# Performance work log

Hardware: AMD Instinct MI355X
Metric: run time of the kernel (lower is better)

The kernel has to match this reference:

```python
import jax, jax.numpy as jnp
import numpy as np

B, A, C, G = 32, 8732, 201, 50
NEG_TO_POS_RATIO = 3
MIN_NEG_SAMPLES = 0
DET_W, VAL_W = 0.5, 0.5
BOX_W = (10.0, 10.0, 5.0, 5.0)  # torchvision SSD BoxCoder weights


def _rand_boxes(key, shape_prefix):
    k1, k2 = jax.random.split(key)
    cxcy = jax.random.uniform(k1, shape_prefix + (2,)) * 300.0
    wh = jax.random.uniform(k2, shape_prefix + (2,)) * 90.0 + 10.0
    return jnp.concatenate([cxcy - 0.5 * wh, cxcy + 0.5 * wh], axis=-1)


def setup_inputs() -> dict:
    key = jax.random.key(0)
    ks = jax.random.split(key, 8)
    boxes = _rand_boxes(ks[0], (B, G))
    labels = jax.random.randint(ks[1], (B, G), 1, C, dtype=jnp.int32)  # foreground labels > 0
    image_label = jax.random.randint(ks[2], (B,), 0, 2, dtype=jnp.int32)
    bbox_regression = jax.random.normal(ks[3], (B, A, 4), dtype=jnp.float32)
    cls_logits = jax.random.normal(ks[4], (B, A, C), dtype=jnp.float32)
    rejection_logits = jax.random.normal(ks[5], (B, 2), dtype=jnp.float32)
    anchors = _rand_boxes(ks[6], (B, A))
    k7a, k7b = jax.random.split(ks[7])
    fg = jax.random.uniform(k7a, (B, A)) < 0.02
    gt_idx = jax.random.randint(k7b, (B, A), 0, G, dtype=jnp.int32)
    matched_idxs = jnp.where(fg, gt_idx, -1).astype(jnp.int32)
    return {"boxes": boxes, "labels": labels, "image_label": image_label,
            "bbox_regression": bbox_regression, "cls_logits": cls_logits,
            "rejection_logits": rejection_logits, "anchors": anchors,
            "matched_idxs": matched_idxs}


def _encode(gt, anc):
    # torchvision BoxCoder.encode_single with weights (10,10,5,5); boxes are xyxy
    aw = anc[..., 2] - anc[..., 0]
    ah = anc[..., 3] - anc[..., 1]
    acx = anc[..., 0] + 0.5 * aw
    acy = anc[..., 1] + 0.5 * ah
    gw = gt[..., 2] - gt[..., 0]
    gh = gt[..., 3] - gt[..., 1]
    gcx = gt[..., 0] + 0.5 * gw
    gcy = gt[..., 1] + 0.5 * gh
    wx, wy, ww, wh = BOX_W
    return jnp.stack([wx * (gcx - acx) / aw,
                      wy * (gcy - acy) / ah,
                      ww * jnp.log(gw / aw),
                      wh * jnp.log(gh / ah)], axis=-1)


def _forward(boxes, bbox_regression, cls_logits, rejection_logits, anchors,
             labels, image_label, matched_idxs):
    fg = matched_idxs >= 0                                  # [B,A]
    safe = jnp.clip(matched_idxs, 0)                        # in-range gather idx
    num_foreground = fg.sum()

    mg_boxes = jnp.take_along_axis(boxes, safe[..., None], axis=1)  # [B,A,4]
    target_reg = _encode(mg_boxes, anchors)
    d = bbox_regression - target_reg
    ad = jnp.abs(d)
    sl1 = jnp.where(ad < 1.0, 0.5 * d * d, ad - 0.5)        # beta=1.0
    bbox_loss = jnp.sum(sl1 * fg[..., None].astype(sl1.dtype), axis=(1, 2))  # [B]

    # --- classification targets + per-anchor CE ---
    cls_targets = jnp.where(fg, jnp.take_along_axis(labels, safe, axis=1), 0)  # [B,A]
    logp = jax.nn.log_softmax(cls_logits, axis=-1)
    cls_loss = -jnp.take_along_axis(logp, cls_targets[..., None], axis=-1)[..., 0]  # [B,A]

    # --- hard negative mining via double-argsort ranking ---
    fg_mask = cls_targets > 0
    num_neg = NEG_TO_POS_RATIO * fg_mask.sum(axis=1, keepdims=True)
    num_neg = jnp.where(num_neg == 0, MIN_NEG_SAMPLES, num_neg)
    neg_loss = jnp.where(fg_mask, -jnp.inf, cls_loss)
    rank = jnp.argsort(jnp.argsort(-neg_loss, axis=1), axis=1)  # descending rank
    bg_mask = rank < num_neg

    N = jnp.maximum(1, num_foreground).astype(cls_loss.dtype)
    images_without_boxes = (cls_targets.sum(axis=1) == 0).sum()
    N_neg = (MIN_NEG_SAMPLES * images_without_boxes).astype(cls_loss.dtype)

    regression_loss = bbox_loss.sum() / N
    classification_loss = (jnp.sum(jnp.where(fg_mask, cls_loss, 0.0)) +
                           jnp.sum(jnp.where(bg_mask, cls_loss, 0.0))) / (N + N_neg)

    # --- validation head loss ---
    val_logp = jax.nn.log_softmax(rejection_logits, axis=-1)
    validation_loss = -jnp.take_along_axis(val_logp, image_label[:, None], axis=-1).mean()

    loss = DET_W * (regression_loss + classification_loss) + VAL_W * validation_loss
    return jnp.stack([loss, regression_loss, classification_loss, validation_loss])


def reference(boxes, labels, image_label, bbox_regression, cls_logits,
              rejection_logits, anchors, matched_idxs):
    return _forward(boxes, bbox_regression, cls_logits, rejection_logits, anchors,
                    labels, image_label, matched_idxs)
```

## Files before the change

### kernel.cpp

```cpp
#include <hip/hip_runtime.h>
#include <math.h>

#define Bn 32
#define An 8732
#define Cn 201
#define Gn 50

#define APB 16
#define CLS_BLOCKS ((An + APB - 1) / APB)
#define LOG2E 1.44269504088896340736f

__device__ __forceinline__ unsigned int f2key(float f) {
    unsigned int u = __float_as_uint(f);
    return (u & 0x80000000u) ? ~u : (u | 0x80000000u);
}
__device__ __forceinline__ float key2f(unsigned int k) {
    return (k & 0x80000000u) ? __uint_as_float(k & 0x7FFFFFFFu) : __uint_as_float(~k);
}
__device__ __forceinline__ float smooth_l1(float d) {
    float ad = fabsf(d);
    return ad < 1.0f ? 0.5f * d * d : ad - 0.5f;
}

#define FGKEY 0x007FFFFFu

__global__ __launch_bounds__(256) void cls_kernel(
        const float* __restrict__ cls_logits,
        const int*   __restrict__ matched_idxs,
        const int*   __restrict__ labels,
        const float* __restrict__ boxes,
        const float* __restrict__ anchors,
        const float* __restrict__ bbox_regression,
        float* __restrict__ neg_loss,
        float* __restrict__ part_cls,
        float* __restrict__ part_box) {
    __shared__ float shc[4], shb[4];
    int b   = blockIdx.y;
    int grp = threadIdx.x >> 4;
    int sub = threadIdx.x & 15;
    int a   = blockIdx.x * APB + grp;
    bool valid = (a < An);
    size_t row = (size_t)b * An + a;

    float my_cl = 0.f, my_box = 0.f;
    if (valid) {
        const float* lg = cls_logits + row * (size_t)Cn;
        float v[13];
        #pragma unroll
        for (int j = 0; j < 12; ++j) v[j] = lg[sub + 16 * j];
        v[12] = (sub < Cn - 192) ? lg[sub + 192] : -INFINITY;

        float mx = v[0];
        #pragma unroll
        for (int j = 1; j < 13; ++j) mx = fmaxf(mx, v[j]);
        #pragma unroll
        for (int off = 8; off; off >>= 1) mx = fmaxf(mx, __shfl_xor(mx, off, 64));

        float s = 0.f;
        #pragma unroll
        for (int j = 0; j < 13; ++j) s += exp2f((v[j] - mx) * LOG2E);
        #pragma unroll
        for (int off = 8; off; off >>= 1) s += __shfl_xor(s, off, 64);

        if (sub == 0) {
            float lse = mx + logf(s);
            int   mi  = matched_idxs[row];
            bool  fg  = (mi >= 0);
            int   t   = fg ? labels[b * Gn + mi] : 0;
            float cl  = lse - lg[t];
            if (fg) {
                neg_loss[row] = -INFINITY;
                my_cl = cl;
                const float* gt = boxes           + (size_t)(b * Gn + mi) * 4;
                const float* an = anchors         + row * 4;
                const float* rg = bbox_regression + row * 4;
                float aw  = an[2] - an[0], ah  = an[3] - an[1];
                float acx = an[0] + 0.5f * aw, acy = an[1] + 0.5f * ah;
                float gw  = gt[2] - gt[0], gh  = gt[3] - gt[1];
                float gcx = gt[0] + 0.5f * gw, gcy = gt[1] + 0.5f * gh;
                float t0 = 10.f * (gcx - acx) / aw;
                float t1 = 10.f * (gcy - acy) / ah;
                float t2 = 5.f * logf(gw / aw);
                float t3 = 5.f * logf(gh / ah);
                my_box = smooth_l1(rg[0] - t0) + smooth_l1(rg[1] - t1)
                       + smooth_l1(rg[2] - t2) + smooth_l1(rg[3] - t3);
            } else {
                neg_loss[row] = cl;
            }
        }
    }
    my_cl  += __shfl_xor(my_cl, 16, 64);  my_cl  += __shfl_xor(my_cl, 32, 64);
    my_box += __shfl_xor(my_box, 16, 64); my_box += __shfl_xor(my_box, 32, 64);
    int wv = threadIdx.x >> 6, lane = threadIdx.x & 63;
    if (lane == 0) { shc[wv] = my_cl; shb[wv] = my_box; }
    __syncthreads();
    if (threadIdx.x == 0) {
        part_cls[b * CLS_BLOCKS + blockIdx.x] = shc[0] + shc[1] + shc[2] + shc[3];
        part_box[b * CLS_BLOCKS + blockIdx.x] = shb[0] + shb[1] + shb[2] + shb[3];
    }
}

#define MIT 9
__global__ __launch_bounds__(1024) void mining_kernel(
        const float* __restrict__ neg_loss,
        const float* __restrict__ part_cls,
        const float* __restrict__ part_box,
        int*   __restrict__ fg_count,
        float* __restrict__ fg_cls_sum,
        float* __restrict__ bbox_sum,
        float* __restrict__ topk_batch) {
    int b    = blockIdx.x;
    int tid  = threadIdx.x;
    int lane = tid & 63;
    int wv   = tid >> 6;
    __shared__ int   h[256];
    __shared__ float wfa[16], wfb[16];
    __shared__ int   wia[16];
    __shared__ unsigned int sh_prefix;
    __shared__ int sh_krem, sh_k;

    const float* vals = neg_loss + (size_t)b * An;
    unsigned int key[MIT];
    int myfg = 0;
    #pragma unroll
    for (int j = 0; j < MIT; ++j) {
        int i = tid + j * 1024;
        unsigned int kk = 0u;
        if (i < An) { kk = f2key(vals[i]); myfg += (kk == FGKEY); }
        key[j] = kk;
    }
    float mc = (tid < CLS_BLOCKS) ? part_cls[b * CLS_BLOCKS + tid] : 0.f;
    float mb = (tid < CLS_BLOCKS) ? part_box[b * CLS_BLOCKS + tid] : 0.f;
    #pragma unroll
    for (int off = 32; off; off >>= 1) {
        mc   += __shfl_xor(mc, off, 64);
        mb   += __shfl_xor(mb, off, 64);
        myfg += __shfl_xor(myfg, off, 64);
    }
    if (lane == 0) { wfa[wv] = mc; wfb[wv] = mb; wia[wv] = myfg; }
    if (tid < 256) h[tid] = 0;
    __syncthreads();
    if (tid == 0) {
        float cs = 0.f, bs = 0.f; int fc = 0;
        for (int i = 0; i < 16; ++i) { cs += wfa[i]; bs += wfb[i]; fc += wia[i]; }
        fg_count[b] = fc; fg_cls_sum[b] = cs; bbox_sum[b] = bs;
        int k = 3 * fc, nneg = An - fc;
        if (k > nneg) k = nneg;
        sh_k = k; sh_krem = k; sh_prefix = 0u;
    }
    __syncthreads();
    int k = sh_k;
    if (k <= 0) { if (tid == 0) topk_batch[b] = 0.f; return; }

    unsigned int prefix = 0; int krem = k;
    for (int p = 0; p < 4; ++p) {
        int shift = 24 - 8 * p;
        #pragma unroll
        for (int j = 0; j < MIT; ++j) {
            unsigned int u = key[j];
            bool match = (p == 0) || ((u >> (shift + 8)) == prefix);
            if (match) atomicAdd(&h[(u >> shift) & 255], 1);
        }
        __syncthreads();
        if (wv == 0) {
            int b0 = 252 - 4 * lane;
            int c0 = h[b0], c1 = h[b0 + 1], c2 = h[b0 + 2], c3 = h[b0 + 3];
            int local = c0 + c1 + c2 + c3;
            int inc = local;
            #pragma unroll
            for (int off = 1; off < 64; off <<= 1) {
                int n = __shfl_up(inc, off, 64);
                if (lane >= off) inc += n;
            }
            unsigned long long m = __ballot(inc >= krem);
            int sel = __ffsll(m) - 1;
            if (lane == sel) {
                int prev = inc - local;
                int digit, above;
                if      (prev + c3 >= krem)           { digit = b0 + 3; above = prev; }
                else if (prev + c3 + c2 >= krem)      { digit = b0 + 2; above = prev + c3; }
                else if (prev + c3 + c2 + c1 >= krem) { digit = b0 + 1; above = prev + c3 + c2; }
                else                                  { digit = b0;     above = prev + c3 + c2 + c1; }
                sh_prefix = (prefix << 8) | (unsigned int)digit;
                sh_krem   = krem - above;
            }
        }
        __syncthreads();
        prefix = sh_prefix; krem = sh_krem;
        if (p < 3) {
            if (tid < 256) h[tid] = 0;
            __syncthreads();
        }
    }

    unsigned int T = prefix;
    float fs = 0.f; int cgt = 0;
    #pragma unroll
    for (int j = 0; j < MIT; ++j)
        if (key[j] > T) { fs += key2f(key[j]); cgt++; }
    #pragma unroll
    for (int off = 32; off; off >>= 1) {
        fs  += __shfl_xor(fs,  off, 64);
        cgt += __shfl_xor(cgt, off, 64);
    }
    if (lane == 0) { wfa[wv] = fs; wia[wv] = cgt; }
    __syncthreads();
    if (tid == 0) {
        float s = 0.f; int c = 0;
        for (int i = 0; i < 16; ++i) { s += wfa[i]; c += wia[i]; }
        topk_batch[b] = s + (float)(k - c) * key2f(T);
    }
}

__global__ void finalize_kernel(
        const int*   __restrict__ fg_count,
        const float* __restrict__ fg_cls_sum,
        const float* __restrict__ bbox_sum,
        const float* __restrict__ topk_batch,
        const float* __restrict__ rejection_logits,
        const int*   __restrict__ image_label,
        float* __restrict__ out) {
    int lane = threadIdx.x;
    int   fc = (lane < Bn) ? fg_count[lane]   : 0;
    float tk = (lane < Bn) ? topk_batch[lane] : 0.f;
    float cs = (lane < Bn) ? fg_cls_sum[lane] : 0.f;
    float bs = (lane < Bn) ? bbox_sum[lane]   : 0.f;
    float vl = 0.f;
    if (lane < Bn) {
        float r0 = rejection_logits[lane * 2];
        float r1 = rejection_logits[lane * 2 + 1];
        float m  = fmaxf(r0, r1);
        float lse = m + logf(expf(r0 - m) + expf(r1 - m));
        vl = lse - ((image_label[lane] == 0) ? r0 : r1);
    }
    #pragma unroll
    for (int off = 32; off; off >>= 1) {
        fc += __shfl_xor(fc, off, 64);
        tk += __shfl_xor(tk, off, 64);
        cs += __shfl_xor(cs, off, 64);
        bs += __shfl_xor(bs, off, 64);
        vl += __shfl_xor(vl, off, 64);
    }
    if (lane == 0) {
        float N   = (float)((fc > 1) ? fc : 1);
        float reg = bs / N;
        float cls = (cs + tk) / N;
        float val = vl / (float)Bn;
        float loss = 0.5f * (reg + cls) + 0.5f * val;
        out[0] = loss; out[1] = reg; out[2] = cls; out[3] = val;
    }
}

extern "C" void kernel_launch(void* const* d_in, const int* in_sizes, int n_in,
                              void* d_out, int out_size, void* d_ws, size_t ws_size,
                              hipStream_t stream) {
    const float* boxes            = (const float*)d_in[0];
    const int*   labels           = (const int*)  d_in[1];
    const int*   image_label      = (const int*)  d_in[2];
    const float* bbox_regression  = (const float*)d_in[3];
    const float* cls_logits       = (const float*)d_in[4];
    const float* rejection_logits = (const float*)d_in[5];
    const float* anchors          = (const float*)d_in[6];
    const int*   matched_idxs     = (const int*)  d_in[7];
    float* out = (float*)d_out;

    float* neg_loss   = (float*)d_ws;
    float* part_cls   = neg_loss + (size_t)Bn * An;
    float* part_box   = part_cls + Bn * CLS_BLOCKS;
    int*   fg_count   = (int*)(part_box + Bn * CLS_BLOCKS);
    float* fg_cls_sum = (float*)(fg_count + Bn);
    float* bbox_sum   = fg_cls_sum + Bn;
    float* topk_batch = bbox_sum + Bn;

    dim3 grid(CLS_BLOCKS, Bn);
    cls_kernel<<<grid, 256, 0, stream>>>(cls_logits, matched_idxs, labels,
                                         boxes, anchors, bbox_regression,
                                         neg_loss, part_cls, part_box);

    mining_kernel<<<Bn, 1024, 0, stream>>>(neg_loss, part_cls, part_box,
                                           fg_count, fg_cls_sum, bbox_sum, topk_batch);

    finalize_kernel<<<1, 64, 0, stream>>>(fg_count, fg_cls_sum, bbox_sum, topk_batch,
                                          rejection_logits, image_label, out);
}
```

Measured before the change: 334.5 us.

## Fuse finalize into mining kernel via last-block counter and privatize histograms

```diff
diff --git a/kernel.cpp b/kernel.cpp
--- a/kernel.cpp
+++ b/kernel.cpp
@@ -33,7 +33,8 @@
         const float* __restrict__ bbox_regression,
         float* __restrict__ neg_loss,
         float* __restrict__ part_cls,
-        float* __restrict__ part_box) {
+        float* __restrict__ part_box,
+        int*   __restrict__ done_counter) {
     __shared__ float shc[4], shb[4];
     int b   = blockIdx.y;
     int grp = threadIdx.x >> 4;
@@ -42,6 +43,9 @@
     bool valid = (a < An);
     size_t row = (size_t)b * An + a;
 
+    if (blockIdx.x == 0 && b == 0 && threadIdx.x == 0)
+        *done_counter = 0;
+
     float my_cl = 0.f, my_box = 0.f;
     if (valid) {
         const float* lg = cls_logits + row * (size_t)Cn;
@@ -66,8 +70,7 @@
             float lse = mx + logf(s);
             int   mi  = matched_idxs[row];
             bool  fg  = (mi >= 0);
-            int   t   = fg ? labels[b * Gn + mi] : 0;
-            float cl  = lse - lg[t];
+            float cl  = lse - (fg ? lg[labels[b * Gn + mi]] : v[0]);
             if (fg) {
                 neg_loss[row] = -INFINITY;
                 my_cl = cl;
@@ -101,6 +104,7 @@
 }
 
 #define MIT 9
+#define HPAD 260
 __global__ __launch_bounds__(1024) void mining_kernel(
         const float* __restrict__ neg_loss,
         const float* __restrict__ part_cls,
@@ -108,16 +112,21 @@
         int*   __restrict__ fg_count,
         float* __restrict__ fg_cls_sum,
         float* __restrict__ bbox_sum,
-        float* __restrict__ topk_batch) {
+        float* __restrict__ topk_batch,
+        int*   __restrict__ done_counter,
+        const float* __restrict__ rejection_logits,
+        const int*   __restrict__ image_label,
+        float* __restrict__ out) {
     int b    = blockIdx.x;
     int tid  = threadIdx.x;
     int lane = tid & 63;
     int wv   = tid >> 6;
-    __shared__ int   h[256];
+    __shared__ int   priv[16 * HPAD];
+    __shared__ int   comb[256];
     __shared__ float wfa[16], wfb[16];
     __shared__ int   wia[16];
     __shared__ unsigned int sh_prefix;
-    __shared__ int sh_krem, sh_k;
+    __shared__ int sh_krem, sh_k, sh_last;
 
     const float* vals = neg_loss + (size_t)b * An;
     unsigned int key[MIT];
@@ -138,116 +147,123 @@
         myfg += __shfl_xor(myfg, off, 64);
     }
     if (lane == 0) { wfa[wv] = mc; wfb[wv] = mb; wia[wv] = myfg; }
-    if (tid < 256) h[tid] = 0;
+    for (int i = tid; i < 16 * HPAD; i += 1024) priv[i] = 0;
     __syncthreads();
     if (tid == 0) {
         float cs = 0.f, bs = 0.f; int fc = 0;
         for (int i = 0; i < 16; ++i) { cs += wfa[i]; bs += wfb[i]; fc += wia[i]; }
-        fg_count[b] = fc; fg_cls_sum[b] = cs; bbox_sum[b] = bs;
+        __hip_atomic_store(&fg_count[b],   fc, __ATOMIC_RELAXED, __HIP_MEMORY_SCOPE_AGENT);
+        __hip_atomic_store(&fg_cls_sum[b], cs, __ATOMIC_RELAXED, __HIP_MEMORY_SCOPE_AGENT);
+        __hip_atomic_store(&bbox_sum[b],   bs, __ATOMIC_RELAXED, __HIP_MEMORY_SCOPE_AGENT);
         int k = 3 * fc, nneg = An - fc;
         if (k > nneg) k = nneg;
-        sh_k = k; sh_krem = k; sh_prefix = 0u;
+        sh_k = k;
     }
     __syncthreads();
     int k = sh_k;
-    if (k <= 0) { if (tid == 0) topk_batch[b] = 0.f; return; }
-
-    unsigned int prefix = 0; int krem = k;
-    for (int p = 0; p < 4; ++p) {
-        int shift = 24 - 8 * p;
-        #pragma unroll
-        for (int j = 0; j < MIT; ++j) {
-            unsigned int u = key[j];
-            bool match = (p == 0) || ((u >> (shift + 8)) == prefix);
-            if (match) atomicAdd(&h[(u >> shift) & 255], 1);
-        }
+    float result = 0.f;
+
+    if (k > 0) {
+        unsigned int prefix = 0; int krem = k;
+        for (int p = 0; p < 4; ++p) {
+            int shift = 24 - 8 * p;
+            int* ph = &priv[wv * HPAD];
+            #pragma unroll
+            for (int j = 0; j < MIT; ++j) {
+                unsigned int u = key[j];
+                bool match = (p == 0) || ((u >> (shift + 8)) == prefix);
+                if (match) atomicAdd(&ph[(u >> shift) & 255], 1);
+            }
+            __syncthreads();
+            if (tid < 256) {
+                int s = 0;
+                #pragma unroll
+                for (int w = 0; w < 16; ++w) { s += priv[w * HPAD + tid]; priv[w * HPAD + tid] = 0; }
+                comb[tid] = s;
+            }
+            __syncthreads();
+            if (wv == 0) {
+                int b0 = 252 - 4 * lane;
+                int c0 = comb[b0], c1 = comb[b0 + 1], c2 = comb[b0 + 2], c3 = comb[b0 + 3];
+                int local = c0 + c1 + c2 + c3;
+                int inc = local;
+                #pragma unroll
+                for (int off = 1; off < 64; off <<= 1) {
+                    int n = __shfl_up(inc, off, 64);
+                    if (lane >= off) inc += n;
+                }
+                unsigned long long m = __ballot(inc >= krem);
+                int sel = __ffsll(m) - 1;
+                if (lane == sel) {
+                    int prev = inc - local;
+                    int digit, above;
+                    if      (prev + c3 >= krem)           { digit = b0 + 3; above = prev; }
+                    else if (prev + c3 + c2 >= krem)      { digit = b0 + 2; above = prev + c3; }
+                    else if (prev + c3 + c2 + c1 >= krem) { digit = b0 + 1; above = prev + c3 + c2; }
+                    else                                  { digit = b0;     above = prev + c3 + c2 + c1; }
+                    sh_prefix = (prefix << 8) | (unsigned int)digit;
+                    sh_krem   = krem - above;
+                }
+            }
+            __syncthreads();
+            prefix = sh_prefix; krem = sh_krem;
+        }
+
+        unsigned int T = prefix;
+        float fs = 0.f; int cgt = 0;
+        #pragma unroll
+        for (int j = 0; j < MIT; ++j)
+            if (key[j] > T) { fs += key2f(key[j]); cgt++; }
+        #pragma unroll
+        for (int off = 32; off; off >>= 1) {
+            fs  += __shfl_xor(fs,  off, 64);
+            cgt += __shfl_xor(cgt, off, 64);
+        }
+        if (lane == 0) { wfa[wv] = fs; wia[wv] = cgt; }
         __syncthreads();
-        if (wv == 0) {
-            int b0 = 252 - 4 * lane;
-            int c0 = h[b0], c1 = h[b0 + 1], c2 = h[b0 + 2], c3 = h[b0 + 3];
-            int local = c0 + c1 + c2 + c3;
-            int inc = local;
-            #pragma unroll
-            for (int off = 1; off < 64; off <<= 1) {
-                int n = __shfl_up(inc, off, 64);
-                if (lane >= off) inc += n;
-            }
-            unsigned long long m = __ballot(inc >= krem);
-            int sel = __ffsll(m) - 1;
-            if (lane == sel) {
-                int prev = inc - local;
-                int digit, above;
-                if      (prev + c3 >= krem)           { digit = b0 + 3; above = prev; }
-                else if (prev + c3 + c2 >= krem)      { digit = b0 + 2; above = prev + c3; }
-                else if (prev + c3 + c2 + c1 >= krem) { digit = b0 + 1; above = prev + c3 + c2; }
-                else                                  { digit = b0;     above = prev + c3 + c2 + c1; }
-                sh_prefix = (prefix << 8) | (unsigned int)digit;
-                sh_krem   = krem - above;
-            }
-        }
-        __syncthreads();
-        prefix = sh_prefix; krem = sh_krem;
-        if (p < 3) {
-            if (tid < 256) h[tid] = 0;
-            __syncthreads();
-        }
-    }
-
-    unsigned int T = prefix;
-    float fs = 0.f; int cgt = 0;
-    #pragma unroll
-    for (int j = 0; j < MIT; ++j)
-        if (key[j] > T) { fs += key2f(key[j]); cgt++; }
-    #pragma unroll
-    for (int off = 32; off; off >>= 1) {
-        fs  += __shfl_xor(fs,  off, 64);
-        cgt += __shfl_xor(cgt, off, 64);
-    }
-    if (lane == 0) { wfa[wv] = fs; wia[wv] = cgt; }
+        if (tid == 0) {
+            float s = 0.f; int c = 0;
+            for (int i = 0; i < 16; ++i) { s += wfa[i]; c += wia[i]; }
+            result = s + (float)(k - c) * key2f(T);
+        }
+    }
+
+    if (tid == 0) {
+        __hip_atomic_store(&topk_batch[b], result, __ATOMIC_RELAXED, __HIP_MEMORY_SCOPE_AGENT);
+        int old = __hip_atomic_fetch_add(done_counter, 1, __ATOMIC_ACQ_REL, __HIP_MEMORY_SCOPE_AGENT);
+        sh_last = (old == Bn - 1);
+    }
     __syncthreads();
-    if (tid == 0) {
-        float s = 0.f; int c = 0;
-        for (int i = 0; i < 16; ++i) { s += wfa[i]; c += wia[i]; }
-        topk_batch[b] = s + (float)(k - c) * key2f(T);
-    }
-}
-
-__global__ void finalize_kernel(
-        const int*   __restrict__ fg_count,
-        const float* __restrict__ fg_cls_sum,
-        const float* __restrict__ bbox_sum,
-        const float* __restrict__ topk_batch,
-        const float* __restrict__ rejection_logits,
-        const int*   __restrict__ image_label,
-        float* __restrict__ out) {
-    int lane = threadIdx.x;
-    int   fc = (lane < Bn) ? fg_count[lane]   : 0;
-    float tk = (lane < Bn) ? topk_batch[lane] : 0.f;
-    float cs = (lane < Bn) ? fg_cls_sum[lane] : 0.f;
-    float bs = (lane < Bn) ? bbox_sum[lane]   : 0.f;
-    float vl = 0.f;
-    if (lane < Bn) {
-        float r0 = rejection_logits[lane * 2];
-        float r1 = rejection_logits[lane * 2 + 1];
-        float m  = fmaxf(r0, r1);
-        float lse = m + logf(expf(r0 - m) + expf(r1 - m));
-        vl = lse - ((image_label[lane] == 0) ? r0 : r1);
-    }
-    #pragma unroll
-    for (int off = 32; off; off >>= 1) {
-        fc += __shfl_xor(fc, off, 64);
-        tk += __shfl_xor(tk, off, 64);
-        cs += __shfl_xor(cs, off, 64);
-        bs += __shfl_xor(bs, off, 64);
-        vl += __shfl_xor(vl, off, 64);
-    }
-    if (lane == 0) {
-        float N   = (float)((fc > 1) ? fc : 1);
-        float reg = bs / N;
-        float cls = (cs + tk) / N;
-        float val = vl / (float)Bn;
-        float loss = 0.5f * (reg + cls) + 0.5f * val;
-        out[0] = loss; out[1] = reg; out[2] = cls; out[3] = val;
+    if (sh_last && tid < 64) {
+        int l = tid;
+        int   fc = 0; float tk = 0.f, cs = 0.f, bs = 0.f, vl = 0.f;
+        if (l < Bn) {
+            fc = __hip_atomic_load(&fg_count[l],   __ATOMIC_RELAXED, __HIP_MEMORY_SCOPE_AGENT);
+            tk = __hip_atomic_load(&topk_batch[l], __ATOMIC_RELAXED, __HIP_MEMORY_SCOPE_AGENT);
+            cs = __hip_atomic_load(&fg_cls_sum[l], __ATOMIC_RELAXED, __HIP_MEMORY_SCOPE_AGENT);
+            bs = __hip_atomic_load(&bbox_sum[l],   __ATOMIC_RELAXED, __HIP_MEMORY_SCOPE_AGENT);
+            float r0 = rejection_logits[l * 2];
+            float r1 = rejection_logits[l * 2 + 1];
+            float m  = fmaxf(r0, r1);
+            float lse = m + logf(expf(r0 - m) + expf(r1 - m));
+            vl = lse - ((image_label[l] == 0) ? r0 : r1);
+        }
+        #pragma unroll
+        for (int off = 32; off; off >>= 1) {
+            fc += __shfl_xor(fc, off, 64);
+            tk += __shfl_xor(tk, off, 64);
+            cs += __shfl_xor(cs, off, 64);
+            bs += __shfl_xor(bs, off, 64);
+            vl += __shfl_xor(vl, off, 64);
+        }
+        if (l == 0) {
+            float N   = (float)((fc > 1) ? fc : 1);
+            float reg = bs / N;
+            float cls = (cs + tk) / N;
+            float val = vl / (float)Bn;
+            out[0] = 0.5f * (reg + cls) + 0.5f * val;
+            out[1] = reg; out[2] = cls; out[3] = val;
+        }
     }
 }
 
@@ -271,15 +287,14 @@
     float* fg_cls_sum = (float*)(fg_count + Bn);
     float* bbox_sum   = fg_cls_sum + Bn;
     float* topk_batch = bbox_sum + Bn;
+    int*   done_ctr   = (int*)(topk_batch + Bn);
 
     dim3 grid(CLS_BLOCKS, Bn);
     cls_kernel<<<grid, 256, 0, stream>>>(cls_logits, matched_idxs, labels,
                                          boxes, anchors, bbox_regression,
-                                         neg_loss, part_cls, part_box);
+                                         neg_loss, part_cls, part_box, done_ctr);
 
     mining_kernel<<<Bn, 1024, 0, stream>>>(neg_loss, part_cls, part_box,
-                                           fg_count, fg_cls_sum, bbox_sum, topk_batch);
-
-    finalize_kernel<<<1, 64, 0, stream>>>(fg_count, fg_cls_sum, bbox_sum, topk_batch,
-                                          rejection_logits, image_label, out);
-}
+                                           fg_count, fg_cls_sum, bbox_sum, topk_batch,
+                                           done_ctr, rejection_logits, image_label, out);
+}
```

Result: no change. 331.0 us (median of 2 runs) (-1.0%).
